# Kernel optimization log

Measured on AMD Instinct MI355X. Metric: run time of the kernel, lower is better.

## Reference

```python
import jax, jax.numpy as jnp
import numpy as np

B, N, K = 32, 8192, 256   # batch_size, mux_in, mux_out
TEMP = 1.0                # Gumbel-softmax temperature
MEM_PENALTY = -1000.0     # penalty for already-sampled elements


def setup_inputs() -> dict:
    key = jax.random.key(0)
    k1, k2 = jax.random.split(key)
    logits = jax.random.normal(k1, (B, N), dtype=jnp.float32)
    # Gumbel(0,1) noise, one draw per (batch, mux_in), repeated over mux_out
    u = jax.random.uniform(k2, (B, N), dtype=jnp.float32, minval=1e-6, maxval=1.0 - 1e-6)
    noise = -jnp.log(-jnp.log(u))
    sample_memory = jnp.zeros((B, N), dtype=jnp.float32)
    return {"logits": logits, "noise": noise, "sample_memory": sample_memory}


def reference(logits, noise, sample_memory):
    # perturbed logits, identical across the K (mux_out) axis -> keep as [B, N]
    perturbed = logits + noise + sample_memory * MEM_PENALTY  # [B, N]

    # top-K selection (straight-through hard path)
    _, topk_idx = jax.lax.top_k(perturbed, K)  # [B, K]
    b_idx = jnp.arange(B)[:, None]             # [B, 1]
    k_idx = jnp.arange(K)[None, :]             # [1, K]

    hard = jnp.zeros((B, N), logits.dtype).at[b_idx, topk_idx].set(1.0)
    hard = hard + sample_memory                # [B, N]

    # masking_matrix: for column k, all elements picked at steps < k are -inf,
    # the element picked at step k is 0 (scatter -inf, cumsum over k, reset to 0)
    M = jnp.zeros((B, N, K), logits.dtype).at[b_idx, topk_idx, k_idx].set(-jnp.inf)
    M = jnp.cumsum(M, axis=2)
    M = M.at[b_idx, topk_idx, k_idx].set(0.0)  # [B, N, K]

    masked = perturbed[:, :, None] + M                         # [B, N, K]
    soft = jax.nn.softmax(masked / TEMP, axis=1).sum(axis=2)   # [B, N]

    # straight-through estimator
    return hard - jax.lax.stop_gradient(soft) + soft
```

## Files before the change

### kernel.cpp

```cpp
#include <hip/hip_runtime.h>


#define NROW 32
#define NCOL 8192
#define KSEL 256
#define THREADS 1024
#define H0S 4097

__device__ __forceinline__ unsigned float_to_key(float f) {
    unsigned u = __float_as_uint(f);
    return (u & 0x80000000u) ? ~u : (u | 0x80000000u);
}

__global__ __launch_bounds__(THREADS) void topk_kernel(
    const float* __restrict__ logits, const float* __restrict__ noise,
    const float* __restrict__ mem, float* __restrict__ out)
{
    __shared__ unsigned hist0[4 * H0S];
    __shared__ __align__(16) unsigned hist1[4096];
    __shared__ unsigned hist2[256];
    __shared__ unsigned wpart[16];
    __shared__ unsigned sh_pn[2];

    const int tid  = threadIdx.x;
    const int wave = tid >> 6;
    const int lane = tid & 63;
    const int grp  = wave >> 2;
    const int base = blockIdx.x * NCOL + tid * 8;

    float4 lg0 = ((const float4*)(logits + base))[0];
    float4 lg1 = ((const float4*)(logits + base))[1];
    float4 no0 = ((const float4*)(noise  + base))[0];
    float4 no1 = ((const float4*)(noise  + base))[1];
    float4 mm0 = ((const float4*)(mem    + base))[0];
    float4 mm1 = ((const float4*)(mem    + base))[1];

    unsigned key[8];
    key[0] = float_to_key(lg0.x + no0.x + mm0.x * -1000.0f);
    key[1] = float_to_key(lg0.y + no0.y + mm0.y * -1000.0f);
    key[2] = float_to_key(lg0.z + no0.z + mm0.z * -1000.0f);
    key[3] = float_to_key(lg0.w + no0.w + mm0.w * -1000.0f);
    key[4] = float_to_key(lg1.x + no1.x + mm1.x * -1000.0f);
    key[5] = float_to_key(lg1.y + no1.y + mm1.y * -1000.0f);
    key[6] = float_to_key(lg1.z + no1.z + mm1.z * -1000.0f);
    key[7] = float_to_key(lg1.w + no1.w + mm1.w * -1000.0f);

#pragma unroll
    for (int i = tid; i < 4 * H0S; i += THREADS) hist0[i] = 0u;
#pragma unroll
    for (int i = tid; i < 4096; i += THREADS) hist1[i] = 0u;
    if (tid < 256) hist2[tid] = 0u;
    __syncthreads();

    {
        unsigned* h0 = hist0 + grp * H0S;
#pragma unroll
        for (int i = 0; i < 8; ++i) atomicAdd(&h0[key[i] >> 20], 1u);
    }
    __syncthreads();

    unsigned need = KSEL;
    unsigned p12, p24;
    const int dbase = 4095 - 4 * tid;

    {
        unsigned c[4], tot = 0;
#pragma unroll
        for (int j = 0; j < 4; ++j) {
            const int d = dbase - j;
            c[j] = hist0[d] + hist0[H0S + d] + hist0[2 * H0S + d] + hist0[3 * H0S + d];
            tot += c[j];
        }
        unsigned s = tot;
#pragma unroll
        for (int off = 1; off < 64; off <<= 1) {
            unsigned nv = __shfl_up(s, off, 64);
            if (lane >= off) s += nv;
        }
        if (lane == 63) wpart[wave] = s;
        __syncthreads();
        unsigned add = 0;
        for (int w = 0; w < wave; ++w) add += wpart[w];
        unsigned cum = s + add - tot;
#pragma unroll
        for (int j = 0; j < 4; ++j) {
            unsigned nc = cum + c[j];
            if (nc >= need && cum < need) {
                sh_pn[0] = (unsigned)(dbase - j);
                sh_pn[1] = need - cum;
            }
            cum = nc;
        }
    }
    __syncthreads();
    p12 = sh_pn[0]; need = sh_pn[1];

#pragma unroll
    for (int i = 0; i < 8; ++i)
        if ((key[i] >> 20) == p12)
            atomicAdd(&hist1[(key[i] >> 8) & 4095u], 1u);
    __syncthreads();

    {
        uint4 v = *(const uint4*)&hist1[dbase - 3];
        unsigned c[4] = {v.w, v.z, v.y, v.x};
        unsigned tot = c[0] + c[1] + c[2] + c[3];
        unsigned s = tot;
#pragma unroll
        for (int off = 1; off < 64; off <<= 1) {
            unsigned nv = __shfl_up(s, off, 64);
            if (lane >= off) s += nv;
        }
        if (lane == 63) wpart[wave] = s;
        __syncthreads();
        unsigned add = 0;
        for (int w = 0; w < wave; ++w) add += wpart[w];
        unsigned cum = s + add - tot;
#pragma unroll
        for (int j = 0; j < 4; ++j) {
            unsigned nc = cum + c[j];
            if (nc >= need && cum < need) {
                sh_pn[0] = (unsigned)(dbase - j);
                sh_pn[1] = need - cum;
            }
            cum = nc;
        }
    }
    __syncthreads();
    p24 = (p12 << 12) | sh_pn[0]; need = sh_pn[1];

#pragma unroll
    for (int i = 0; i < 8; ++i)
        if ((key[i] >> 8) == p24)
            atomicAdd(&hist2[key[i] & 255u], 1u);
    __syncthreads();

    if (wave == 0) {
        const int d0 = 255 - 4 * lane;
        unsigned c0 = hist2[d0], c1 = hist2[d0 - 1],
                 c2 = hist2[d0 - 2], c3 = hist2[d0 - 3];
        unsigned tot = c0 + c1 + c2 + c3, s = tot;
#pragma unroll
        for (int off = 1; off < 64; off <<= 1) {
            unsigned nv = __shfl_up(s, off, 64);
            if (lane >= off) s += nv;
        }
        unsigned P = s - tot;
        unsigned cum0 = P + c0, cum1 = cum0 + c1, cum2 = cum1 + c2, cum3 = cum2 + c3;
        if (cum0 >= need && P < need)         { sh_pn[0] = (unsigned)d0;       sh_pn[1] = need - P;    }
        else if (cum1 >= need && cum0 < need) { sh_pn[0] = (unsigned)(d0 - 1); sh_pn[1] = need - cum0; }
        else if (cum2 >= need && cum1 < need) { sh_pn[0] = (unsigned)(d0 - 2); sh_pn[1] = need - cum1; }
        else if (cum3 >= need && cum2 < need) { sh_pn[0] = (unsigned)(d0 - 3); sh_pn[1] = need - cum2; }
    }
    __syncthreads();
    const unsigned T     = (p24 << 8) | sh_pn[0];
    const unsigned needF = sh_pn[1];

    unsigned local_eq = 0;
#pragma unroll
    for (int i = 0; i < 8; ++i) local_eq += (key[i] == T) ? 1u : 0u;
    unsigned s2 = local_eq;
#pragma unroll
    for (int off = 1; off < 64; off <<= 1) {
        unsigned nv = __shfl_up(s2, off, 64);
        if (lane >= off) s2 += nv;
    }
    if (lane == 63) wpart[wave] = s2;
    __syncthreads();
    unsigned rank = s2 - local_eq;
    for (int w = 0; w < wave; ++w) rank += wpart[w];

    float o[8];
#pragma unroll
    for (int i = 0; i < 8; ++i) {
        float sel;
        if (key[i] > T)       sel = 1.0f;
        else if (key[i] == T) { sel = (rank < needF) ? 1.0f : 0.0f; ++rank; }
        else                  sel = 0.0f;
        o[i] = sel;
    }
    o[0] += mm0.x; o[1] += mm0.y; o[2] += mm0.z; o[3] += mm0.w;
    o[4] += mm1.x; o[5] += mm1.y; o[6] += mm1.z; o[7] += mm1.w;
    ((float4*)(out + base))[0] = make_float4(o[0], o[1], o[2], o[3]);
    ((float4*)(out + base))[1] = make_float4(o[4], o[5], o[6], o[7]);
}

extern "C" void kernel_launch(void* const* d_in, const int* in_sizes, int n_in,
                              void* d_out, int out_size, void* d_ws, size_t ws_size,
                              hipStream_t stream) {
    const float* logits = (const float*)d_in[0];
    const float* noise  = (const float*)d_in[1];
    const float* mem    = (const float*)d_in[2];
    float* out = (float*)d_out;

    topk_kernel<<<NROW, THREADS, 0, stream>>>(logits, noise, mem, out);
}
```

Before: 64.38 us.

## Split radix top-k into chunked histogram pass and per-row selection pass

Splits the single 32-block kernel into two launches. The first runs 256 blocks, one per 1024-element chunk of a row; each computes the perturbed keys, writes them to workspace, and writes a 12-bit prefix histogram packed as 16-bit counts. The second runs one block per row, sums the eight chunk histograms, and then runs the remaining radix refinement and output as before. This aims to spread the load and first-histogram work across more compute units than the 32 the original could occupy. The cost is a second launch plus a round trip of keys and histograms through global memory. The old kernel is kept as a fallback when the workspace is too small.

```diff
diff --git a/kernel.cpp b/kernel.cpp
--- a/kernel.cpp
+++ b/kernel.cpp
@@ -4,12 +4,212 @@
 #define NROW 32
 #define NCOL 8192
 #define KSEL 256
+#define NCHUNK 8
+#define CHUNK 1024
+#define T1 256
 #define THREADS 1024
 #define H0S 4097
 
 __device__ __forceinline__ unsigned float_to_key(float f) {
     unsigned u = __float_as_uint(f);
     return (u & 0x80000000u) ? ~u : (u | 0x80000000u);
+}
+
+__global__ __launch_bounds__(T1) void topk_pass1(
+    const float* __restrict__ logits, const float* __restrict__ noise,
+    const float* __restrict__ mem, unsigned* __restrict__ wskeys,
+    unsigned short* __restrict__ wshist)
+{
+    __shared__ __align__(16) unsigned h[4096];
+    const int tid = threadIdx.x;
+    const int r = blockIdx.x >> 3;
+    const int c = blockIdx.x & 7;
+    const int base = r * NCOL + c * CHUNK + tid * 4;
+
+    float4 lg = *(const float4*)(logits + base);
+    float4 no = *(const float4*)(noise + base);
+    float4 mm = *(const float4*)(mem + base);
+
+    unsigned ka = float_to_key(lg.x + no.x + mm.x * -1000.0f);
+    unsigned kb = float_to_key(lg.y + no.y + mm.y * -1000.0f);
+    unsigned kc = float_to_key(lg.z + no.z + mm.z * -1000.0f);
+    unsigned kd = float_to_key(lg.w + no.w + mm.w * -1000.0f);
+
+    *(uint4*)(wskeys + base) = make_uint4(ka, kb, kc, kd);
+
+    const uint4 z = make_uint4(0u, 0u, 0u, 0u);
+#pragma unroll
+    for (int i = 0; i < 4; ++i) ((uint4*)h)[tid + 256 * i] = z;
+    __syncthreads();
+
+    atomicAdd(&h[ka >> 20], 1u);
+    atomicAdd(&h[kb >> 20], 1u);
+    atomicAdd(&h[kc >> 20], 1u);
+    atomicAdd(&h[kd >> 20], 1u);
+    __syncthreads();
+
+    uint4 q0 = ((const uint4*)h)[4 * tid + 0];
+    uint4 q1 = ((const uint4*)h)[4 * tid + 1];
+    uint4 q2 = ((const uint4*)h)[4 * tid + 2];
+    uint4 q3 = ((const uint4*)h)[4 * tid + 3];
+    uint4 w0 = make_uint4(q0.x | (q0.y << 16), q0.z | (q0.w << 16),
+                          q1.x | (q1.y << 16), q1.z | (q1.w << 16));
+    uint4 w1 = make_uint4(q2.x | (q2.y << 16), q2.z | (q2.w << 16),
+                          q3.x | (q3.y << 16), q3.z | (q3.w << 16));
+    uint4* outh = (uint4*)(wshist + (size_t)(r * NCHUNK + c) * 4096);
+    outh[2 * tid]     = w0;
+    outh[2 * tid + 1] = w1;
+}
+
+__global__ __launch_bounds__(THREADS) void topk_pass2(
+    const unsigned* __restrict__ wskeys, const unsigned short* __restrict__ wshist,
+    const float* __restrict__ mem, float* __restrict__ out)
+{
+    __shared__ __align__(16) unsigned hist1[4096];
+    __shared__ __align__(16) unsigned hist2[256];
+    __shared__ unsigned wpart[16];
+    __shared__ unsigned sh_pn[2];
+
+    const int tid  = threadIdx.x;
+    const int wave = tid >> 6;
+    const int lane = tid & 63;
+    const int r    = blockIdx.x;
+    const int base = r * NCOL + tid * 8;
+    const int dbase = 4095 - 4 * tid;
+
+    uint4 kv0 = ((const uint4*)(wskeys + base))[0];
+    uint4 kv1 = ((const uint4*)(wskeys + base))[1];
+    float4 mm0 = ((const float4*)(mem + base))[0];
+    float4 mm1 = ((const float4*)(mem + base))[1];
+    unsigned key[8] = {kv0.x, kv0.y, kv0.z, kv0.w, kv1.x, kv1.y, kv1.z, kv1.w};
+
+    ((uint4*)hist1)[tid] = make_uint4(0u, 0u, 0u, 0u);
+    if (tid < 64) ((uint4*)hist2)[tid] = make_uint4(0u, 0u, 0u, 0u);
+
+    unsigned c0 = 0, c1 = 0, c2 = 0, c3 = 0;
+#pragma unroll
+    for (int cc = 0; cc < NCHUNK; ++cc) {
+        uint2 v = *(const uint2*)(wshist + (size_t)(r * NCHUNK + cc) * 4096 + (dbase - 3));
+        c3 += v.x & 0xffffu; c2 += v.x >> 16;
+        c1 += v.y & 0xffffu; c0 += v.y >> 16;
+    }
+
+    unsigned need = KSEL;
+    unsigned p12, p24;
+    {
+        unsigned c[4] = {c0, c1, c2, c3};
+        unsigned tot = c0 + c1 + c2 + c3, s = tot;
+#pragma unroll
+        for (int off = 1; off < 64; off <<= 1) {
+            unsigned nv = __shfl_up(s, off, 64);
+            if (lane >= off) s += nv;
+        }
+        if (lane == 63) wpart[wave] = s;
+        __syncthreads();
+        unsigned add = 0;
+        for (int w = 0; w < wave; ++w) add += wpart[w];
+        unsigned cum = s + add - tot;
+#pragma unroll
+        for (int j = 0; j < 4; ++j) {
+            unsigned nc = cum + c[j];
+            if (nc >= need && cum < need) {
+                sh_pn[0] = (unsigned)(dbase - j);
+                sh_pn[1] = need - cum;
+            }
+            cum = nc;
+        }
+    }
+    __syncthreads();
+    p12 = sh_pn[0]; need = sh_pn[1];
+
+#pragma unroll
+    for (int i = 0; i < 8; ++i)
+        if ((key[i] >> 20) == p12)
+            atomicAdd(&hist1[(key[i] >> 8) & 4095u], 1u);
+    __syncthreads();
+
+    {
+        uint4 v = *(const uint4*)&hist1[dbase - 3];
+        unsigned c[4] = {v.w, v.z, v.y, v.x};
+        unsigned tot = c[0] + c[1] + c[2] + c[3];
+        unsigned s = tot;
+#pragma unroll
+        for (int off = 1; off < 64; off <<= 1) {
+            unsigned nv = __shfl_up(s, off, 64);
+            if (lane >= off) s += nv;
+        }
+        if (lane == 63) wpart[wave] = s;
+        __syncthreads();
+        unsigned add = 0;
+        for (int w = 0; w < wave; ++w) add += wpart[w];
+        unsigned cum = s + add - tot;
+#pragma unroll
+        for (int j = 0; j < 4; ++j) {
+            unsigned nc = cum + c[j];
+            if (nc >= need && cum < need) {
+                sh_pn[0] = (unsigned)(dbase - j);
+                sh_pn[1] = need - cum;
+            }
+            cum = nc;
+        }
+    }
+    __syncthreads();
+    p24 = (p12 << 12) | sh_pn[0]; need = sh_pn[1];
+
+#pragma unroll
+    for (int i = 0; i < 8; ++i)
+        if ((key[i] >> 8) == p24)
+            atomicAdd(&hist2[key[i] & 255u], 1u);
+    __syncthreads();
+
+    if (wave == 0) {
+        const int d0 = 255 - 4 * lane;
+        unsigned e0 = hist2[d0], e1 = hist2[d0 - 1],
+                 e2 = hist2[d0 - 2], e3 = hist2[d0 - 3];
+        unsigned tot = e0 + e1 + e2 + e3, s = tot;
+#pragma unroll
+        for (int off = 1; off < 64; off <<= 1) {
+            unsigned nv = __shfl_up(s, off, 64);
+            if (lane >= off) s += nv;
+        }
+        unsigned P = s - tot;
+        unsigned cum0 = P + e0, cum1 = cum0 + e1, cum2 = cum1 + e2, cum3 = cum2 + e3;
+        if (cum0 >= need && P < need)         { sh_pn[0] = (unsigned)d0;       sh_pn[1] = need - P;    }
+        else if (cum1 >= need && cum0 < need) { sh_pn[0] = (unsigned)(d0 - 1); sh_pn[1] = need - cum0; }
+        else if (cum2 >= need && cum1 < need) { sh_pn[0] = (unsigned)(d0 - 2); sh_pn[1] = need - cum1; }
+        else if (cum3 >= need && cum2 < need) { sh_pn[0] = (unsigned)(d0 - 3); sh_pn[1] = need - cum2; }
+    }
+    __syncthreads();
+    const unsigned T     = (p24 << 8) | sh_pn[0];
+    const unsigned needF = sh_pn[1];
+
+    unsigned local_eq = 0;
+#pragma unroll
+    for (int i = 0; i < 8; ++i) local_eq += (key[i] == T) ? 1u : 0u;
+    unsigned s2 = local_eq;
+#pragma unroll
+    for (int off = 1; off < 64; off <<= 1) {
+        unsigned nv = __shfl_up(s2, off, 64);
+        if (lane >= off) s2 += nv;
+    }
+    if (lane == 63) wpart[wave] = s2;
+    __syncthreads();
+    unsigned rank = s2 - local_eq;
+    for (int w = 0; w < wave; ++w) rank += wpart[w];
+
+    float o[8];
+#pragma unroll
+    for (int i = 0; i < 8; ++i) {
+        float sel;
+        if (key[i] > T)       sel = 1.0f;
+        else if (key[i] == T) { sel = (rank < needF) ? 1.0f : 0.0f; ++rank; }
+        else                  sel = 0.0f;
+        o[i] = sel;
+    }
+    o[0] += mm0.x; o[1] += mm0.y; o[2] += mm0.z; o[3] += mm0.w;
+    o[4] += mm1.x; o[5] += mm1.y; o[6] += mm1.z; o[7] += mm1.w;
+    ((float4*)(out + base))[0] = make_float4(o[0], o[1], o[2], o[3]);
+    ((float4*)(out + base))[1] = make_float4(o[4], o[5], o[6], o[7]);
 }
 
 __global__ __launch_bounds__(THREADS) void topk_kernel(
@@ -137,16 +337,16 @@
 
     if (wave == 0) {
         const int d0 = 255 - 4 * lane;
-        unsigned c0 = hist2[d0], c1 = hist2[d0 - 1],
-                 c2 = hist2[d0 - 2], c3 = hist2[d0 - 3];
-        unsigned tot = c0 + c1 + c2 + c3, s = tot;
+        unsigned e0 = hist2[d0], e1 = hist2[d0 - 1],
+                 e2 = hist2[d0 - 2], e3 = hist2[d0 - 3];
+        unsigned tot = e0 + e1 + e2 + e3, s = tot;
 #pragma unroll
         for (int off = 1; off < 64; off <<= 1) {
             unsigned nv = __shfl_up(s, off, 64);
             if (lane >= off) s += nv;
         }
         unsigned P = s - tot;
-        unsigned cum0 = P + c0, cum1 = cum0 + c1, cum2 = cum1 + c2, cum3 = cum2 + c3;
+        unsigned cum0 = P + e0, cum1 = cum0 + e1, cum2 = cum1 + e2, cum3 = cum2 + e3;
         if (cum0 >= need && P < need)         { sh_pn[0] = (unsigned)d0;       sh_pn[1] = need - P;    }
         else if (cum1 >= need && cum0 < need) { sh_pn[0] = (unsigned)(d0 - 1); sh_pn[1] = need - cum0; }
         else if (cum2 >= need && cum1 < need) { sh_pn[0] = (unsigned)(d0 - 2); sh_pn[1] = need - cum1; }
@@ -193,5 +393,15 @@
     const float* mem    = (const float*)d_in[2];
     float* out = (float*)d_out;
 
-    topk_kernel<<<NROW, THREADS, 0, stream>>>(logits, noise, mem, out);
+    const size_t keys_bytes = (size_t)NROW * NCOL * sizeof(unsigned);
+    const size_t hist_bytes = (size_t)NROW * NCHUNK * 4096 * sizeof(unsigned short);
+
+    if (ws_size >= keys_bytes + hist_bytes) {
+        unsigned* wskeys = (unsigned*)d_ws;
+        unsigned short* wshist = (unsigned short*)((char*)d_ws + keys_bytes);
+        topk_pass1<<<NROW * NCHUNK, T1, 0, stream>>>(logits, noise, mem, wskeys, wshist);
+        topk_pass2<<<NROW, THREADS, 0, stream>>>(wskeys, wshist, mem, out);
+    } else {
+        topk_kernel<<<NROW, THREADS, 0, stream>>>(logits, noise, mem, out);
+    }
 }
```

After: 66.89 us. 1.04x slower.
